# Performance work log

Hardware: AMD Instinct MI355X
Metric: run time of the kernel (lower is better)

## Reference

```python
import jax, jax.numpy as jnp
import numpy as np

N_USER = 50000
N_ITEM = 50000
E = 500000
L = 100000
F = 128
HID = 128
OUT = 64


def setup_inputs() -> dict:
    key = jax.random.key(0)
    ks = jax.random.split(key, 21)

    def ei(k, n_src, n_dst, n):
        return jnp.stack([
            jax.random.randint(jax.random.fold_in(k, 0), (n,), 0, n_src, dtype=jnp.int32),
            jax.random.randint(jax.random.fold_in(k, 1), (n,), 0, n_dst, dtype=jnp.int32),
        ])

    s1 = 1.0 / np.sqrt(F)
    s2 = 1.0 / np.sqrt(HID)
    inp = {
        "x_user": jax.random.normal(ks[0], (N_USER, F), jnp.float32),
        "x_item": jax.random.normal(ks[1], (N_ITEM, F), jnp.float32),
        "W1_src": jax.random.normal(ks[2], (3, F, HID), jnp.float32) * s1,
        "W1_dst": jax.random.normal(ks[3], (3, F, HID), jnp.float32) * s1,
        "a1_src": jax.random.normal(ks[4], (3, HID), jnp.float32) * s2,
        "a1_dst": jax.random.normal(ks[5], (3, HID), jnp.float32) * s2,
        "b1": jax.random.normal(ks[6], (3, HID), jnp.float32) * 0.01,
        "W2_src": jax.random.normal(ks[7], (3, HID, OUT), jnp.float32) * s2,
        "W2_dst": jax.random.normal(ks[8], (3, HID, OUT), jnp.float32) * s2,
        "a2_src": jax.random.normal(ks[9], (3, OUT), jnp.float32) * (1.0 / np.sqrt(OUT)),
        "a2_dst": jax.random.normal(ks[10], (3, OUT), jnp.float32) * (1.0 / np.sqrt(OUT)),
        "b2": jax.random.normal(ks[11], (3, OUT), jnp.float32) * 0.01,
        "rel_w": jax.random.normal(ks[12], (3, OUT), jnp.float32),
        "ei_rates": ei(ks[13], N_USER, N_ITEM, E),
        "ei_rev": ei(ks[14], N_ITEM, N_USER, E),
        "ei_follows": ei(ks[15], N_USER, N_USER, E),
        "eli_rates": ei(ks[16], N_USER, N_ITEM, L),
        "eli_rev": ei(ks[17], N_ITEM, N_USER, L),
        "eli_follows": ei(ks[18], N_USER, N_USER, L),
    }
    return inp


def _leaky(x):
    return jnp.where(x > 0, x, 0.2 * x)


def _gat(x_src, x_dst, ei, Ws, Wd, a_s, a_d, b, n_dst):
    # Single-head GATConv: linear src/dst, additive attention, segment softmax over dst.
    h_src = x_src @ Ws          # [Ns, C]
    h_dst = x_dst @ Wd          # [Nd, C]
    src, dst = ei[0], ei[1]
    logits = _leaky((h_src @ a_s)[src] + (h_dst @ a_d)[dst])  # [E]
    m = jax.ops.segment_max(logits, dst, num_segments=n_dst)
    m = jnp.where(jnp.isfinite(m), m, 0.0)
    ex = jnp.exp(logits - m[dst])
    den = jax.ops.segment_sum(ex, dst, num_segments=n_dst)
    alpha = ex / (den[dst] + 1e-16)
    out = jax.ops.segment_sum(alpha[:, None] * h_src[src], dst, num_segments=n_dst)
    return out + b


def reference(x_user, x_item, W1_src, W1_dst, a1_src, a1_dst, b1,
              W2_src, W2_dst, a2_src, a2_dst, b2, rel_w,
              ei_rates, ei_rev, ei_follows, eli_rates, eli_rev, eli_follows):
    # Layer 1 (HeteroConv sums contributions into each dst node type)
    h_item = _gat(x_user, x_item, ei_rates, W1_src[0], W1_dst[0], a1_src[0], a1_dst[0], b1[0], N_ITEM)
    h_user = (_gat(x_item, x_user, ei_rev, W1_src[1], W1_dst[1], a1_src[1], a1_dst[1], b1[1], N_USER)
              + _gat(x_user, x_user, ei_follows, W1_src[2], W1_dst[2], a1_src[2], a1_dst[2], b1[2], N_USER))
    h_item = jax.nn.relu(h_item)
    h_user = jax.nn.relu(h_user)
    # Layer 2
    o_item = _gat(h_user, h_item, ei_rates, W2_src[0], W2_dst[0], a2_src[0], a2_dst[0], b2[0], N_ITEM)
    o_user = (_gat(h_item, h_user, ei_rev, W2_src[1], W2_dst[1], a2_src[1], a2_dst[1], b2[1], N_USER)
              + _gat(h_user, h_user, ei_follows, W2_src[2], W2_dst[2], a2_src[2], a2_dst[2], b2[2], N_USER))
    # Bilinear edge scoring per relation
    p0 = jnp.sum(o_user[eli_rates[0]] * rel_w[0] * o_item[eli_rates[1]], axis=-1)
    p1 = jnp.sum(o_item[eli_rev[0]] * rel_w[1] * o_user[eli_rev[1]], axis=-1)
    p2 = jnp.sum(o_user[eli_follows[0]] * rel_w[2] * o_user[eli_follows[1]], axis=-1)
    return jnp.stack([p0, p1, p2])  # [3, L]
```

## Files before the change

kernel.cpp:

```cpp
#include <hip/hip_runtime.h>
#include <cstdint>
#include <cstddef>

#define N_NODE 50000
#define NEDGE  500000
#define NL     100000
#define FDIM   128
#define HIDD   128
#define OUTD   64
#define NBSC   98
#define NB     49
#define BCH    8192
#define NBP1   62

typedef unsigned int uint32;
typedef unsigned short ushort16;
typedef __attribute__((ext_vector_type(8))) short bf16x8;
typedef __attribute__((ext_vector_type(4))) float f32x4;

__device__ __forceinline__ float leakyf(float x) { return x > 0.f ? x : 0.2f * x; }

__device__ __forceinline__ uint32 bf16r(float x) {
    uint32 u = __float_as_uint(x);
    return (u + 0x7fffu + ((u >> 16) & 1u)) >> 16;
}
__device__ __forceinline__ float bf_lo(uint32 u) { return __uint_as_float(u << 16); }
__device__ __forceinline__ float bf_hi(uint32 u) { return __uint_as_float(u & 0xffff0000u); }

__global__ void fold_wd(const float* __restrict__ W1d, const float* __restrict__ a1d,
                        const float* __restrict__ W2d, const float* __restrict__ a2d,
                        float* __restrict__ wd1, float* __restrict__ wd2) {
    int r = blockIdx.x;
    int f = threadIdx.x;
    const float* w  = W1d + ((size_t)r * FDIM + f) * HIDD;
    const float* a  = a1d + r * HIDD;
    float s = 0.f;
    for (int h = 0; h < HIDD; ++h) s += w[h] * a[h];
    wd1[r * FDIM + f] = s;
    const float* w2 = W2d + ((size_t)r * HIDD + f) * OUTD;
    const float* a2 = a2d + r * OUTD;
    float s2 = 0.f;
    for (int o = 0; o < OUTD; ++o) s2 += w2[o] * a2[o];
    wd2[r * HIDD + f] = s2;
}

__global__ void wt_k(const float* __restrict__ W1s, const float* __restrict__ W2s,
                     ushort16* __restrict__ WT1, ushort16* __restrict__ WT2) {
    int idx = blockIdx.x * 256 + threadIdx.x;
    if (blockIdx.y == 0) {
        if (idx < 3 * FDIM * HIDD) {
            int k = idx & 127, n = (idx >> 7) & 127, r = idx >> 14;
            WT1[idx] = (ushort16)bf16r(W1s[((size_t)r * FDIM + k) * HIDD + n]);
        }
    } else {
        if (idx < 3 * HIDD * OUTD) {
            int k = idx & 127, n = (idx >> 7) & 63, r = idx >> 13;
            WT2[idx] = (ushort16)bf16r(W2s[((size_t)r * HIDD + k) * OUTD + n]);
        }
    }
}


__global__ __launch_bounds__(256) void part_hist(const int* __restrict__ e0,
                                                 const int* __restrict__ e1,
                                                 const int* __restrict__ e2,
                                                 int* __restrict__ bh) {
    int r = blockIdx.y, t = threadIdx.x;
    const int* ei  = (r == 0) ? e0 : (r == 1) ? e1 : e2;
    const int* dst = ei + NEDGE;
    __shared__ int lh[NB];
    if (t < NB) lh[t] = 0;
    __syncthreads();
    int base = blockIdx.x * BCH;
    int lim  = base + BCH; if (lim > NEDGE) lim = NEDGE;
    for (int i = base + t; i < lim; i += 256)
        atomicAdd(&lh[dst[i] >> 10], 1);
    __syncthreads();
    if (t < NB) bh[((size_t)r * NB + t) * NBP1 + blockIdx.x] = lh[t];
}

__global__ __launch_bounds__(256) void part_scan(int* __restrict__ bh,
                                                 int* __restrict__ bkbase) {
    int r = blockIdx.x, t = threadIdx.x;
    int* a = bh + (size_t)r * NB * NBP1;
    const int n = NB * NBP1;
    const int per = (n + 255) / 256;
    int lo = t * per, hi = lo + per; if (hi > n) hi = n;
    int s = 0;
    for (int i = lo; i < hi; ++i) s += a[i];
    __shared__ int sm[256];
    sm[t] = s;
    __syncthreads();
    for (int off = 1; off < 256; off <<= 1) {
        int x = (t >= off) ? sm[t - off] : 0;
        __syncthreads();
        sm[t] += x;
        __syncthreads();
    }
    int run = sm[t] - s;
    for (int i = lo; i < hi; ++i) { int c = a[i]; a[i] = run; run += c; }
    __syncthreads();
    if (t < NB) bkbase[r * (NB + 1) + t] = a[t * NBP1];
    if (t == NB) bkbase[r * (NB + 1) + NB] = NEDGE;
}

__global__ __launch_bounds__(256) void part_scatter(const int* __restrict__ e0,
                                                    const int* __restrict__ e1,
                                                    const int* __restrict__ e2,
                                                    const int* __restrict__ bh,
                                                    int2* __restrict__ bucketed) {
    int r = blockIdx.y, t = threadIdx.x;
    const int* ei  = (r == 0) ? e0 : (r == 1) ? e1 : e2;
    const int* dst = ei + NEDGE;
    __shared__ int cur[NB];
    if (t < NB) cur[t] = bh[((size_t)r * NB + t) * NBP1 + blockIdx.x];
    __syncthreads();
    int2* bk = bucketed + (size_t)r * NEDGE;
    int base = blockIdx.x * BCH;
    int lim  = base + BCH; if (lim > NEDGE) lim = NEDGE;
    for (int i = base + t; i < lim; i += 256) {
        int d = dst[i], s_ = ei[i];
        int pos = atomicAdd(&cur[d >> 10], 1);
        bk[pos] = make_int2(s_, d);
    }
}

__global__ __launch_bounds__(256) void bucket_count(const int2* __restrict__ bucketed,
                                                    const int* __restrict__ bkbase,
                                                    int* __restrict__ counts_all) {
    int r = blockIdx.y, k = blockIdx.x, t = threadIdx.x;
    int s0 = bkbase[r * (NB + 1) + k], s1 = bkbase[r * (NB + 1) + k + 1];
    __shared__ int lh[1024];
#pragma unroll
    for (int i = 0; i < 4; ++i) lh[t + i * 256] = 0;
    __syncthreads();
    const int2* bk = bucketed + (size_t)r * NEDGE;
    for (int i = s0 + t; i < s1; i += 256)
        atomicAdd(&lh[bk[i].y & 1023], 1);
    __syncthreads();
    int gbase = k << 10;
    int* cnt = counts_all + (size_t)r * N_NODE;
#pragma unroll
    for (int i = 0; i < 4; ++i) {
        int idx = t + i * 256;
        if (gbase + idx < N_NODE) cnt[gbase + idx] = lh[idx];
    }
}

__global__ __launch_bounds__(256) void scan1(const int* __restrict__ counts_all,
                                             int* __restrict__ bsum) {
    int r = blockIdx.y, b = blockIdx.x, t = threadIdx.x;
    int base = b * 512;
    int lim = N_NODE - base; if (lim > 512) lim = 512;
    const int* c = counts_all + (size_t)r * N_NODE + base;
    int v0 = (2 * t     < lim) ? c[2 * t]     : 0;
    int v1 = (2 * t + 1 < lim) ? c[2 * t + 1] : 0;
    __shared__ int sm[256];
    sm[t] = v0 + v1;
    __syncthreads();
    for (int off = 128; off; off >>= 1) {
        if (t < off) sm[t] += sm[t + off];
        __syncthreads();
    }
    if (t == 0) bsum[r * NBSC + b] = sm[0];
}

__global__ __launch_bounds__(256) void scan3(const int* __restrict__ counts_all,
                                             int* __restrict__ rowptr_all,
                                             const int* __restrict__ bsum) {
    int r = blockIdx.y, b = blockIdx.x, t = threadIdx.x;
    __shared__ int sm[256];
    sm[t] = (t < b) ? bsum[r * NBSC + t] : 0;
    __syncthreads();
    for (int off = 128; off; off >>= 1) {
        if (t < off) sm[t] += sm[t + off];
        __syncthreads();
    }
    int boff = sm[0];
    __syncthreads();

    int base = b * 512;
    int lim = N_NODE - base; if (lim > 512) lim = 512;
    const int* c = counts_all + (size_t)r * N_NODE;
    int* rp = rowptr_all + (size_t)r * (N_NODE + 1);
    int i0 = base + 2 * t, i1 = i0 + 1;
    int v0 = (2 * t     < lim) ? c[i0] : 0;
    int v1 = (2 * t + 1 < lim) ? c[i1] : 0;
    int ps = v0 + v1;
    sm[t] = ps;
    __syncthreads();
    for (int off = 1; off < 256; off <<= 1) {
        int x = (t >= off) ? sm[t - off] : 0;
        __syncthreads();
        sm[t] += x;
        __syncthreads();
    }
    int excl = sm[t] - ps + boff;
    if (2 * t < lim)     rp[i0] = excl;
    if (2 * t + 1 < lim) rp[i1] = excl + v0;
    if (b == 0 && t == 0) rp[N_NODE] = NEDGE;
}

__global__ __launch_bounds__(256) void bucket_scatter(const int2* __restrict__ bucketed,
                                                      const int* __restrict__ bkbase,
                                                      const int* __restrict__ rowptr_all,
                                                      int* __restrict__ srcs_all) {
    int r = blockIdx.y, k = blockIdx.x, t = threadIdx.x;
    int s0 = bkbase[r * (NB + 1) + k], s1 = bkbase[r * (NB + 1) + k + 1];
    int gbase = k << 10;
    const int* rp = rowptr_all + (size_t)r * (N_NODE + 1);
    __shared__ int cur[1024];
#pragma unroll
    for (int i = 0; i < 4; ++i) {
        int idx = t + i * 256;
        cur[idx] = (gbase + idx < N_NODE) ? rp[gbase + idx] : 0;
    }
    __syncthreads();
    const int2* bk = bucketed + (size_t)r * NEDGE;
    int* out = srcs_all + (size_t)r * NEDGE;
    for (int i = s0 + t; i < s1; i += 256) {
        int2 e = bk[i];
        int pos = atomicAdd(&cur[e.y & 1023], 1);
        out[pos] = e.x;
    }
}

template <int BN, bool RELU, bool DOT>
__global__ __launch_bounds__(256) void gemm_mfma(const float* __restrict__ A0,
                                                 const float* __restrict__ A1,
                                                 const float* __restrict__ A2,
                                                 const ushort16* __restrict__ WTbase,
                                                 const float* __restrict__ avec_base,
                                                 ushort16* __restrict__ Cbase,
                                                 float* __restrict__ al_base,
                                                 const float* __restrict__ wdvec,
                                                 float* __restrict__ adst_base, int M) {
    constexpr int K = 128;
    __shared__ ushort16 aslds[64 * K];
    __shared__ ushort16 bslds[BN * K];
    const int r = blockIdx.y;
    const float* A = (r == 0) ? A0 : (r == 1) ? A1 : A2;
    const int t    = threadIdx.x;
    const int lane = t & 63;
    const int w    = t >> 6;
    const int m0   = blockIdx.x * 64;

    {
        const uint4* src = reinterpret_cast<const uint4*>(WTbase + (size_t)r * BN * K);
        char* bb = reinterpret_cast<char*>(bslds);
#pragma unroll
        for (int i = t; i < BN * 16; i += 256) {
            int n = i >> 4, c16 = i & 15;
            uint32 off = (uint32)(n * 256 + c16 * 16) ^ (uint32)((n & 7) << 4);
            *reinterpret_cast<uint4*>(bb + off) = src[i];
        }
    }
    const float4* A4 = reinterpret_cast<const float4*>(A);
    const int mr = (r == 0) ? 1 : (r == 1) ? 0 : 2;
    const float* wdot = wdvec + mr * K;
    char* ab = reinterpret_cast<char*>(aslds);
    float dp[8];
#pragma unroll
    for (int i = 0; i < 8; ++i) dp[i] = 0.f;
#pragma unroll
    for (int i = 0; i < 8; ++i) {
        int idx = t + i * 256;
        int row = idx >> 5, kq = idx & 31;
        float4 v = make_float4(0.f, 0.f, 0.f, 0.f);
        if (m0 + row < M) {
            v = A4[(size_t)(m0 + row) * 32 + kq];
            if (RELU) {
                v.x = fmaxf(v.x, 0.f); v.y = fmaxf(v.y, 0.f);
                v.z = fmaxf(v.z, 0.f); v.w = fmaxf(v.w, 0.f);
            }
        }
        if (DOT) {
            float4 wv = *reinterpret_cast<const float4*>(&wdot[kq * 4]);
            dp[i] = fmaf(v.x, wv.x, dp[i]); dp[i] = fmaf(v.y, wv.y, dp[i]);
            dp[i] = fmaf(v.z, wv.z, dp[i]); dp[i] = fmaf(v.w, wv.w, dp[i]);
        }
        uint2 p;
        p.x = bf16r(v.x) | (bf16r(v.y) << 16);
        p.y = bf16r(v.z) | (bf16r(v.w) << 16);
        uint32 off = (uint32)(row * 256 + kq * 8) ^ (uint32)((row & 7) << 4);
        *reinterpret_cast<uint2*>(ab + off) = p;
    }
    if (DOT) {
        float* adst = adst_base + (size_t)mr * M;
#pragma unroll
        for (int i = 0; i < 8; ++i) {
            float p = dp[i];
            p += __shfl_xor(p, 16); p += __shfl_xor(p, 8); p += __shfl_xor(p, 4);
            p += __shfl_xor(p, 2);  p += __shfl_xor(p, 1);
            int row = (t + i * 256) >> 5;
            if ((t & 31) == 0 && m0 + row < M) adst[m0 + row] = p;
        }
    }
    __syncthreads();

    const int col0 = lane & 15;
    const int kgrp = lane >> 4;
    const int arow = w * 16 + col0;
    bf16x8 afrag[4];
#pragma unroll
    for (int ks = 0; ks < 4; ++ks) {
        uint32 off = (uint32)(arow * 256 + ks * 64 + kgrp * 16) ^ (uint32)((arow & 7) << 4);
        afrag[ks] = *reinterpret_cast<const bf16x8*>(ab + off);
    }
    constexpr int NT = BN / 16;
    f32x4 acc[NT];
#pragma unroll
    for (int n = 0; n < NT; ++n) acc[n] = (f32x4){0.f, 0.f, 0.f, 0.f};
    const char* bb = reinterpret_cast<const char*>(bslds);
#pragma unroll
    for (int n = 0; n < NT; ++n) {
        int bcol = n * 16 + col0;
        uint32 xw = (uint32)((bcol & 7) << 4);
#pragma unroll
        for (int ks = 0; ks < 4; ++ks) {
            uint32 off = (uint32)(bcol * 256 + ks * 64 + kgrp * 16) ^ xw;
            bf16x8 bfrag = *reinterpret_cast<const bf16x8*>(bb + off);
            acc[n] = __builtin_amdgcn_mfma_f32_16x16x32_bf16(afrag[ks], bfrag, acc[n], 0, 0, 0);
        }
    }

    ushort16* C = Cbase + (size_t)r * M * BN;
    const float* av = avec_base + r * BN;
    const int rbase = m0 + w * 16 + kgrp * 4;
    float p4[4] = {0.f, 0.f, 0.f, 0.f};
#pragma unroll
    for (int n = 0; n < NT; ++n) {
        float asv = av[n * 16 + col0];
#pragma unroll
        for (int reg = 0; reg < 4; ++reg) {
            int rr = rbase + reg;
            if (rr < M) C[(size_t)rr * BN + n * 16 + col0] = (ushort16)bf16r(acc[n][reg]);
            p4[reg] = fmaf(acc[n][reg], asv, p4[reg]);
        }
    }
    float* al = al_base + (size_t)r * M;
#pragma unroll
    for (int reg = 0; reg < 4; ++reg) {
        float q = p4[reg];
        q += __shfl_xor(q, 1); q += __shfl_xor(q, 2);
        q += __shfl_xor(q, 4); q += __shfl_xor(q, 8);
        int rr = rbase + reg;
        if (col0 == 0 && rr < M) al[rr] = q;
    }
}

__device__ __forceinline__ float4 seg128p(const int* __restrict__ rp, const int* __restrict__ ss,
                                          const float* __restrict__ als,
                                          const uint2* __restrict__ hv2,
                                          float ad, int d, int half, int col) {
    int s = rp[d], e = rp[d + 1];
    float den = 0.f;
    float4 ac = make_float4(0.f, 0.f, 0.f, 0.f);
    int i = s;
    for (; i + 4 <= e; i += 4) {
        int sA = ss[i + half];
        int sB = ss[i + 2 + half];
        float lA = als[sA], lB = als[sB];
        uint2 uA = hv2[(size_t)sA * 32 + col];
        uint2 uB = hv2[(size_t)sB * 32 + col];
        float eA = __expf(leakyf(lA + ad));
        float eB = __expf(leakyf(lB + ad));
        den += eA + eB;
        ac.x = fmaf(eA, bf_lo(uA.x), ac.x); ac.y = fmaf(eA, bf_hi(uA.x), ac.y);
        ac.z = fmaf(eA, bf_lo(uA.y), ac.z); ac.w = fmaf(eA, bf_hi(uA.y), ac.w);
        ac.x = fmaf(eB, bf_lo(uB.x), ac.x); ac.y = fmaf(eB, bf_hi(uB.x), ac.y);
        ac.z = fmaf(eB, bf_lo(uB.y), ac.z); ac.w = fmaf(eB, bf_hi(uB.y), ac.w);
    }
    if (i + 2 <= e) {
        int sA = ss[i + half];
        float lA = als[sA];
        uint2 uA = hv2[(size_t)sA * 32 + col];
        float eA = __expf(leakyf(lA + ad));
        den += eA;
        ac.x = fmaf(eA, bf_lo(uA.x), ac.x); ac.y = fmaf(eA, bf_hi(uA.x), ac.y);
        ac.z = fmaf(eA, bf_lo(uA.y), ac.z); ac.w = fmaf(eA, bf_hi(uA.y), ac.w);
        i += 2;
    }
    if (i < e && half == 0) {
        int sA = ss[i];
        float lA = als[sA];
        uint2 uA = hv2[(size_t)sA * 32 + col];
        float eA = __expf(leakyf(lA + ad));
        den += eA;
        ac.x = fmaf(eA, bf_lo(uA.x), ac.x); ac.y = fmaf(eA, bf_hi(uA.x), ac.y);
        ac.z = fmaf(eA, bf_lo(uA.y), ac.z); ac.w = fmaf(eA, bf_hi(uA.y), ac.w);
    }
    den  += __shfl_xor(den, 32);
    ac.x += __shfl_xor(ac.x, 32); ac.y += __shfl_xor(ac.y, 32);
    ac.z += __shfl_xor(ac.z, 32); ac.w += __shfl_xor(ac.w, 32);
    float rden = 1.0f / (den + 1e-16f);
    return make_float4(ac.x * rden, ac.y * rden, ac.z * rden, ac.w * rden);
}

__device__ __forceinline__ float2 seg64p(const int* __restrict__ rp, const int* __restrict__ ss,
                                         const float* __restrict__ als,
                                         const uint32* __restrict__ hv,
                                         float ad, int d, int half, int col) {
    int s = rp[d], e = rp[d + 1];
    float den = 0.f, ax = 0.f, ay = 0.f;
    int i = s;
    for (; i + 4 <= e; i += 4) {
        int sA = ss[i + half];
        int sB = ss[i + 2 + half];
        float lA = als[sA], lB = als[sB];
        uint32 uA = hv[(size_t)sA * 32 + col];
        uint32 uB = hv[(size_t)sB * 32 + col];
        float eA = __expf(leakyf(lA + ad));
        float eB = __expf(leakyf(lB + ad));
        den += eA + eB;
        ax = fmaf(eA, bf_lo(uA), ax); ay = fmaf(eA, bf_hi(uA), ay);
        ax = fmaf(eB, bf_lo(uB), ax); ay = fmaf(eB, bf_hi(uB), ay);
    }
    if (i + 2 <= e) {
        int sA = ss[i + half];
        float lA = als[sA];
        uint32 uA = hv[(size_t)sA * 32 + col];
        float eA = __expf(leakyf(lA + ad));
        den += eA;
        ax = fmaf(eA, bf_lo(uA), ax); ay = fmaf(eA, bf_hi(uA), ay);
        i += 2;
    }
    if (i < e && half == 0) {
        int sA = ss[i];
        float lA = als[sA];
        uint32 uA = hv[(size_t)sA * 32 + col];
        float eA = __expf(leakyf(lA + ad));
        den += eA;
        ax = fmaf(eA, bf_lo(uA), ax); ay = fmaf(eA, bf_hi(uA), ay);
    }
    den += __shfl_xor(den, 32);
    ax  += __shfl_xor(ax, 32);
    ay  += __shfl_xor(ay, 32);
    float rden = 1.0f / (den + 1e-16f);
    return make_float2(ax * rden, ay * rden);
}

__global__ __launch_bounds__(256) void agg1_sp(const int* __restrict__ rowptr_all,
                                               const int* __restrict__ srcs_all,
                                               const float* __restrict__ alsrc_all,
                                               float* __restrict__ aldst_all,
                                               const ushort16* __restrict__ hs_all,
                                               const float* __restrict__ b1,
                                               const float* __restrict__ wd2,
                                               float* __restrict__ h_item,
                                               float* __restrict__ h_user) {
    const int lane = threadIdx.x & 63;
    const int d = blockIdx.x * 4 + (threadIdx.x >> 6);
    if (d >= N_NODE) return;
    const int half = lane >> 5, col = lane & 31;
    const uint2* hv2 = reinterpret_cast<const uint2*>(hs_all);
    if (blockIdx.y == 0) {
        float4 w = seg128p(rowptr_all, srcs_all, alsrc_all, hv2, aldst_all[d], d, half, col);
        float4 b = ((const float4*)b1)[col];
        float4 h = make_float4(w.x + b.x, w.y + b.y, w.z + b.z, w.w + b.w);
        if (half == 0) ((float4*)h_item)[(size_t)d * 32 + col] = h;
        float4 v0 = ((const float4*)wd2)[col];
        float p = fmaxf(h.x, 0.f) * v0.x + fmaxf(h.y, 0.f) * v0.y
                + fmaxf(h.z, 0.f) * v0.z + fmaxf(h.w, 0.f) * v0.w;
        p += __shfl_xor(p, 16); p += __shfl_xor(p, 8);
        p += __shfl_xor(p, 4);  p += __shfl_xor(p, 2); p += __shfl_xor(p, 1);
        if (lane == 0) aldst_all[d] = p;
    } else {
        float4 w1 = seg128p(rowptr_all + (N_NODE + 1), srcs_all + NEDGE,
                            alsrc_all + N_NODE, hv2 + (size_t)N_NODE * 32,
                            aldst_all[N_NODE + d], d, half, col);
        float4 w2 = seg128p(rowptr_all + 2 * (N_NODE + 1), srcs_all + (size_t)2 * NEDGE,
                            alsrc_all + 2 * N_NODE, hv2 + (size_t)2 * N_NODE * 32,
                            aldst_all[2 * N_NODE + d], d, half, col);
        float4 bA = ((const float4*)(b1 + HIDD))[col];
        float4 bB = ((const float4*)(b1 + 2 * HIDD))[col];
        float4 h = make_float4(w1.x + w2.x + bA.x + bB.x, w1.y + w2.y + bA.y + bB.y,
                               w1.z + w2.z + bA.z + bB.z, w1.w + w2.w + bA.w + bB.w);
        if (half == 0) ((float4*)h_user)[(size_t)d * 32 + col] = h;
        float hx = fmaxf(h.x, 0.f), hy = fmaxf(h.y, 0.f);
        float hz = fmaxf(h.z, 0.f), hw = fmaxf(h.w, 0.f);
        float4 v1 = ((const float4*)(wd2 + HIDD))[col];
        float4 v2 = ((const float4*)(wd2 + 2 * HIDD))[col];
        float p1 = hx * v1.x + hy * v1.y + hz * v1.z + hw * v1.w;
        float p2 = hx * v2.x + hy * v2.y + hz * v2.z + hw * v2.w;
        p1 += __shfl_xor(p1, 16); p1 += __shfl_xor(p1, 8);
        p1 += __shfl_xor(p1, 4);  p1 += __shfl_xor(p1, 2); p1 += __shfl_xor(p1, 1);
        p2 += __shfl_xor(p2, 16); p2 += __shfl_xor(p2, 8);
        p2 += __shfl_xor(p2, 4);  p2 += __shfl_xor(p2, 2); p2 += __shfl_xor(p2, 1);
        if (lane == 0) {
            aldst_all[N_NODE + d]     = p1;
            aldst_all[2 * N_NODE + d] = p2;
        }
    }
}

__global__ __launch_bounds__(256) void agg2_sp(const int* __restrict__ rowptr_all,
                                               const int* __restrict__ srcs_all,
                                               const float* __restrict__ alsrc_all,
                                               const float* __restrict__ aldst_all,
                                               const ushort16* __restrict__ hs_all,
                                               const float* __restrict__ b2,
                                               float* __restrict__ o_item,
                                               float* __restrict__ o_user) {
    const int lane = threadIdx.x & 63;
    const int d = blockIdx.x * 4 + (threadIdx.x >> 6);
    if (d >= N_NODE) return;
    const int half = lane >> 5, col = lane & 31;
    const uint32* hv = reinterpret_cast<const uint32*>(hs_all);
    if (blockIdx.y == 0) {
        float2 w = seg64p(rowptr_all, srcs_all, alsrc_all, hv, aldst_all[d], d, half, col);
        float2 b = ((const float2*)b2)[col];
        if (half == 0)
            ((float2*)o_item)[(size_t)d * 32 + col] = make_float2(w.x + b.x, w.y + b.y);
    } else {
        float2 w1 = seg64p(rowptr_all + (N_NODE + 1), srcs_all + NEDGE,
                           alsrc_all + N_NODE, hv + (size_t)N_NODE * 32,
                           aldst_all[N_NODE + d], d, half, col);
        float2 w2 = seg64p(rowptr_all + 2 * (N_NODE + 1), srcs_all + (size_t)2 * NEDGE,
                           alsrc_all + 2 * N_NODE, hv + (size_t)2 * N_NODE * 32,
                           aldst_all[2 * N_NODE + d], d, half, col);
        float2 bA = ((const float2*)(b2 + OUTD))[col];
        float2 bB = ((const float2*)(b2 + 2 * OUTD))[col];
        if (half == 0)
            ((float2*)o_user)[(size_t)d * 32 + col] =
                make_float2(w1.x + w2.x + bA.x + bB.x, w1.y + w2.y + bA.y + bB.y);
    }
}

__global__ void score_k(const int* __restrict__ e0, const int* __restrict__ e1,
                        const int* __restrict__ e2,
                        const float* __restrict__ o_user, const float* __restrict__ o_item,
                        const float* __restrict__ relw, float* __restrict__ out, int L) {
    int g    = blockIdx.x * 4 + (threadIdx.x >> 6);
    int lane = threadIdx.x & 63;
    int r = g / L, l = g - r * L;
    if (r >= 3) return;
    const int* ei = (r == 0) ? e0 : (r == 1) ? e1 : e2;
    int ai = ei[l];
    int bi = ei[L + l];
    const float* A = (r == 1) ? o_item : o_user;
    const float* B = (r == 0) ? o_item : o_user;
    float v = A[(size_t)ai * OUTD + lane] * relw[r * OUTD + lane] * B[(size_t)bi * OUTD + lane];
#pragma unroll
    for (int off = 32; off; off >>= 1) v += __shfl_xor(v, off);
    if (lane == 0) out[r * L + l] = v;
}

extern "C" void kernel_launch(void* const* d_in, const int* in_sizes, int n_in,
                              void* d_out, int out_size, void* d_ws, size_t ws_size,
                              hipStream_t stream) {
    const float* x_user = (const float*)d_in[0];
    const float* x_item = (const float*)d_in[1];
    const float* W1s = (const float*)d_in[2];
    const float* W1d = (const float*)d_in[3];
    const float* a1s = (const float*)d_in[4];
    const float* a1d = (const float*)d_in[5];
    const float* b1  = (const float*)d_in[6];
    const float* W2s = (const float*)d_in[7];
    const float* W2d = (const float*)d_in[8];
    const float* a2s = (const float*)d_in[9];
    const float* a2d = (const float*)d_in[10];
    const float* b2  = (const float*)d_in[11];
    const float* relw= (const float*)d_in[12];
    const int* ei0 = (const int*)d_in[13];
    const int* ei1 = (const int*)d_in[14];
    const int* ei2 = (const int*)d_in[15];
    const int* el0 = (const int*)d_in[16];
    const int* el1 = (const int*)d_in[17];
    const int* el2 = (const int*)d_in[18];
    float* out = (float*)d_out;
    (void)ws_size; (void)n_in; (void)in_sizes; (void)out_size;

    char* ws = (char*)d_ws;
    size_t off = 0;
    auto alloc = [&](size_t bytes) -> void* {
        void* p = ws + off;
        off = (off + bytes + 255) & ~(size_t)255;
        return p;
    };
    int*     rowptr_all = (int*)alloc((size_t)3 * (N_NODE + 1) * 4);
    int*     counts_all = (int*)alloc((size_t)3 * N_NODE * 4);
    int*     srcs_all   = (int*)alloc((size_t)3 * NEDGE * 4);
    int*     bsum       = (int*)alloc((size_t)3 * NBSC * 4);
    int*     bh         = (int*)alloc((size_t)3 * NB * NBP1 * 4);
    int*     bkbase     = (int*)alloc((size_t)3 * (NB + 1) * 4);
    int2*    bucketed   = (int2*)alloc((size_t)3 * NEDGE * 8);
    ushort16* hs_bf     = (ushort16*)alloc((size_t)3 * N_NODE * HIDD * 2);
    ushort16* WT1       = (ushort16*)alloc((size_t)3 * HIDD * FDIM * 2);
    ushort16* WT2       = (ushort16*)alloc((size_t)3 * OUTD * HIDD * 2);
    float*   h_item1    = (float*)alloc((size_t)2 * N_NODE * HIDD * 4);
    float*   h_user1    = h_item1 + (size_t)N_NODE * HIDD;
    float*   o_item     = (float*)alloc((size_t)N_NODE * OUTD * 4);
    float*   o_user     = (float*)alloc((size_t)N_NODE * OUTD * 4);
    float*   alsrc_all  = (float*)alloc((size_t)3 * N_NODE * 4);
    float*   aldst_all  = (float*)alloc((size_t)3 * N_NODE * 4);
    float*   wd1        = (float*)alloc(3 * FDIM * 4);
    float*   wd2        = (float*)alloc(3 * HIDD * 4);

    fold_wd<<<3, 128, 0, stream>>>(W1d, a1d, W2d, a2d, wd1, wd2);
    wt_k<<<dim3(192, 2), 256, 0, stream>>>(W1s, W2s, WT1, WT2);

    part_hist<<<dim3(NBP1, 3), 256, 0, stream>>>(ei0, ei1, ei2, bh);
    part_scan<<<3, 256, 0, stream>>>(bh, bkbase);
    part_scatter<<<dim3(NBP1, 3), 256, 0, stream>>>(ei0, ei1, ei2, bh, bucketed);
    bucket_count<<<dim3(NB, 3), 256, 0, stream>>>(bucketed, bkbase, counts_all);
    scan1<<<dim3(NBSC, 3), 256, 0, stream>>>(counts_all, bsum);
    scan3<<<dim3(NBSC, 3), 256, 0, stream>>>(counts_all, rowptr_all, bsum);
    bucket_scatter<<<dim3(NB, 3), 256, 0, stream>>>(bucketed, bkbase, rowptr_all, srcs_all);

    const int ag = (N_NODE + 3) / 4;
    const int gg = (N_NODE + 63) / 64;

    gemm_mfma<128, false, true><<<dim3(gg, 3), 256, 0, stream>>>(
        x_user, x_item, x_user, WT1, a1s, hs_bf, alsrc_all, wd1, aldst_all, N_NODE);
    agg1_sp<<<dim3(ag, 2), 256, 0, stream>>>(rowptr_all, srcs_all, alsrc_all, aldst_all,
                                             hs_bf, b1, wd2, h_item1, h_user1);

    gemm_mfma<64, true, false><<<dim3(gg, 3), 256, 0, stream>>>(
        h_user1, h_item1, h_user1, WT2, a2s, hs_bf, alsrc_all, wd2, aldst_all, N_NODE);
    agg2_sp<<<dim3(ag, 2), 256, 0, stream>>>(rowptr_all, srcs_all, alsrc_all, aldst_all,
                                             hs_bf, b2, o_item, o_user);

    score_k<<<(3 * NL + 3) / 4, 256, 0, stream>>>(el0, el1, el2, o_user, o_item, relw, out, NL);
}
```

Before: 331.7 us.

## Store intermediate activations in bf16 and pack bucketed edges into 32 bits

The layer-1 outputs (h_item1/h_user1) and the layer-2 outputs (o_item/o_user) are now written as bf16 instead of fp32. The second GEMM reads the bf16 activations directly and applies ReLU on the packed bits, and the score kernel converts bf16 back to float. Edge bucketing packs the source index and the low 10 bits of the destination into one 32-bit word instead of an int2. Together these halve the global memory traffic in several memory-bound stages, at the cost of extra rounding in the final outputs.

```diff
diff --git a/kernel.cpp b/kernel.cpp
--- a/kernel.cpp
+++ b/kernel.cpp
@@ -18,6 +18,8 @@
 typedef __attribute__((ext_vector_type(8))) short bf16x8;
 typedef __attribute__((ext_vector_type(4))) float f32x4;
 
+static_assert(N_NODE < 65536, "src packs into 16 bits");
+
 __device__ __forceinline__ float leakyf(float x) { return x > 0.f ? x : 0.2f * x; }
 
 __device__ __forceinline__ uint32 bf16r(float x) {
@@ -26,6 +28,12 @@
 }
 __device__ __forceinline__ float bf_lo(uint32 u) { return __uint_as_float(u << 16); }
 __device__ __forceinline__ float bf_hi(uint32 u) { return __uint_as_float(u & 0xffff0000u); }
+__device__ __forceinline__ uint32 relu_bf2(uint32 u) {
+    uint32 lo = u & 0xFFFFu, hi = u >> 16;
+    lo = (lo & 0x8000u) ? 0u : lo;
+    hi = (hi & 0x8000u) ? 0u : hi;
+    return lo | (hi << 16);
+}
 
 __global__ void fold_wd(const float* __restrict__ W1d, const float* __restrict__ a1d,
                         const float* __restrict__ W2d, const float* __restrict__ a2d,
@@ -108,24 +116,24 @@
                                                     const int* __restrict__ e1,
                                                     const int* __restrict__ e2,
                                                     const int* __restrict__ bh,
-                                                    int2* __restrict__ bucketed) {
+                                                    uint32* __restrict__ bucketed) {
     int r = blockIdx.y, t = threadIdx.x;
     const int* ei  = (r == 0) ? e0 : (r == 1) ? e1 : e2;
     const int* dst = ei + NEDGE;
     __shared__ int cur[NB];
     if (t < NB) cur[t] = bh[((size_t)r * NB + t) * NBP1 + blockIdx.x];
     __syncthreads();
-    int2* bk = bucketed + (size_t)r * NEDGE;
+    uint32* bk = bucketed + (size_t)r * NEDGE;
     int base = blockIdx.x * BCH;
     int lim  = base + BCH; if (lim > NEDGE) lim = NEDGE;
     for (int i = base + t; i < lim; i += 256) {
         int d = dst[i], s_ = ei[i];
         int pos = atomicAdd(&cur[d >> 10], 1);
-        bk[pos] = make_int2(s_, d);
-    }
-}
-
-__global__ __launch_bounds__(256) void bucket_count(const int2* __restrict__ bucketed,
+        bk[pos] = (uint32)s_ | ((uint32)(d & 1023) << 16);
+    }
+}
+
+__global__ __launch_bounds__(256) void bucket_count(const uint32* __restrict__ bucketed,
                                                     const int* __restrict__ bkbase,
                                                     int* __restrict__ counts_all) {
     int r = blockIdx.y, k = blockIdx.x, t = threadIdx.x;
@@ -134,9 +142,9 @@
 #pragma unroll
     for (int i = 0; i < 4; ++i) lh[t + i * 256] = 0;
     __syncthreads();
-    const int2* bk = bucketed + (size_t)r * NEDGE;
+    const uint32* bk = bucketed + (size_t)r * NEDGE;
     for (int i = s0 + t; i < s1; i += 256)
-        atomicAdd(&lh[bk[i].y & 1023], 1);
+        atomicAdd(&lh[bk[i] >> 16], 1);
     __syncthreads();
     int gbase = k << 10;
     int* cnt = counts_all + (size_t)r * N_NODE;
@@ -201,7 +209,7 @@
     if (b == 0 && t == 0) rp[N_NODE] = NEDGE;
 }
 
-__global__ __launch_bounds__(256) void bucket_scatter(const int2* __restrict__ bucketed,
+__global__ __launch_bounds__(256) void bucket_scatter(const uint32* __restrict__ bucketed,
                                                       const int* __restrict__ bkbase,
                                                       const int* __restrict__ rowptr_all,
                                                       int* __restrict__ srcs_all) {
@@ -216,19 +224,19 @@
         cur[idx] = (gbase + idx < N_NODE) ? rp[gbase + idx] : 0;
     }
     __syncthreads();
-    const int2* bk = bucketed + (size_t)r * NEDGE;
+    const uint32* bk = bucketed + (size_t)r * NEDGE;
     int* out = srcs_all + (size_t)r * NEDGE;
     for (int i = s0 + t; i < s1; i += 256) {
-        int2 e = bk[i];
-        int pos = atomicAdd(&cur[e.y & 1023], 1);
-        out[pos] = e.x;
-    }
-}
-
-template <int BN, bool RELU, bool DOT>
-__global__ __launch_bounds__(256) void gemm_mfma(const float* __restrict__ A0,
-                                                 const float* __restrict__ A1,
-                                                 const float* __restrict__ A2,
+        uint32 e = bk[i];
+        int pos = atomicAdd(&cur[e >> 16], 1);
+        out[pos] = (int)(e & 0xFFFFu);
+    }
+}
+
+template <int BN, bool RELU, bool DOT, bool ABF16>
+__global__ __launch_bounds__(256) void gemm_mfma(const void* __restrict__ A0,
+                                                 const void* __restrict__ A1,
+                                                 const void* __restrict__ A2,
                                                  const ushort16* __restrict__ WTbase,
                                                  const float* __restrict__ avec_base,
                                                  ushort16* __restrict__ Cbase,
@@ -239,7 +247,7 @@
     __shared__ ushort16 aslds[64 * K];
     __shared__ ushort16 bslds[BN * K];
     const int r = blockIdx.y;
-    const float* A = (r == 0) ? A0 : (r == 1) ? A1 : A2;
+    const void* Av = (r == 0) ? A0 : (r == 1) ? A1 : A2;
     const int t    = threadIdx.x;
     const int lane = t & 63;
     const int w    = t >> 6;
@@ -255,45 +263,61 @@
             *reinterpret_cast<uint4*>(bb + off) = src[i];
         }
     }
-    const float4* A4 = reinterpret_cast<const float4*>(A);
-    const int mr = (r == 0) ? 1 : (r == 1) ? 0 : 2;
-    const float* wdot = wdvec + mr * K;
     char* ab = reinterpret_cast<char*>(aslds);
-    float dp[8];
-#pragma unroll
-    for (int i = 0; i < 8; ++i) dp[i] = 0.f;
-#pragma unroll
-    for (int i = 0; i < 8; ++i) {
-        int idx = t + i * 256;
-        int row = idx >> 5, kq = idx & 31;
-        float4 v = make_float4(0.f, 0.f, 0.f, 0.f);
-        if (m0 + row < M) {
-            v = A4[(size_t)(m0 + row) * 32 + kq];
-            if (RELU) {
-                v.x = fmaxf(v.x, 0.f); v.y = fmaxf(v.y, 0.f);
-                v.z = fmaxf(v.z, 0.f); v.w = fmaxf(v.w, 0.f);
+    if (ABF16) {
+        const uint2* A2v = reinterpret_cast<const uint2*>(Av);
+#pragma unroll
+        for (int i = 0; i < 8; ++i) {
+            int idx = t + i * 256;
+            int row = idx >> 5, kq = idx & 31;
+            uint2 p = make_uint2(0u, 0u);
+            if (m0 + row < M) {
+                p = A2v[(size_t)(m0 + row) * 32 + kq];
+                if (RELU) { p.x = relu_bf2(p.x); p.y = relu_bf2(p.y); }
             }
+            uint32 off = (uint32)(row * 256 + kq * 8) ^ (uint32)((row & 7) << 4);
+            *reinterpret_cast<uint2*>(ab + off) = p;
+        }
+    } else {
+        const float4* A4 = reinterpret_cast<const float4*>(Av);
+        const int mr = (r == 0) ? 1 : (r == 1) ? 0 : 2;
+        const float* wdot = wdvec + mr * K;
+        float dp[8];
+#pragma unroll
+        for (int i = 0; i < 8; ++i) dp[i] = 0.f;
+#pragma unroll
+        for (int i = 0; i < 8; ++i) {
+            int idx = t + i * 256;
+            int row = idx >> 5, kq = idx & 31;
+            float4 v = make_float4(0.f, 0.f, 0.f, 0.f);
+            if (m0 + row < M) {
+                v = A4[(size_t)(m0 + row) * 32 + kq];
+                if (RELU) {
+                    v.x = fmaxf(v.x, 0.f); v.y = fmaxf(v.y, 0.f);
+                    v.z = fmaxf(v.z, 0.f); v.w = fmaxf(v.w, 0.f);
+                }
+            }
+            if (DOT) {
+                float4 wv = *reinterpret_cast<const float4*>(&wdot[kq * 4]);
+                dp[i] = fmaf(v.x, wv.x, dp[i]); dp[i] = fmaf(v.y, wv.y, dp[i]);
+                dp[i] = fmaf(v.z, wv.z, dp[i]); dp[i] = fmaf(v.w, wv.w, dp[i]);
+            }
+            uint2 p;
+            p.x = bf16r(v.x) | (bf16r(v.y) << 16);
+            p.y = bf16r(v.z) | (bf16r(v.w) << 16);
+            uint32 off = (uint32)(row * 256 + kq * 8) ^ (uint32)((row & 7) << 4);
+            *reinterpret_cast<uint2*>(ab + off) = p;
         }
         if (DOT) {
-            float4 wv = *reinterpret_cast<const float4*>(&wdot[kq * 4]);
-            dp[i] = fmaf(v.x, wv.x, dp[i]); dp[i] = fmaf(v.y, wv.y, dp[i]);
-            dp[i] = fmaf(v.z, wv.z, dp[i]); dp[i] = fmaf(v.w, wv.w, dp[i]);
-        }
-        uint2 p;
-        p.x = bf16r(v.x) | (bf16r(v.y) << 16);
-        p.y = bf16r(v.z) | (bf16r(v.w) << 16);
-        uint32 off = (uint32)(row * 256 + kq * 8) ^ (uint32)((row & 7) << 4);
-        *reinterpret_cast<uint2*>(ab + off) = p;
-    }
-    if (DOT) {
-        float* adst = adst_base + (size_t)mr * M;
-#pragma unroll
-        for (int i = 0; i < 8; ++i) {
-            float p = dp[i];
-            p += __shfl_xor(p, 16); p += __shfl_xor(p, 8); p += __shfl_xor(p, 4);
-            p += __shfl_xor(p, 2);  p += __shfl_xor(p, 1);
-            int row = (t + i * 256) >> 5;
-            if ((t & 31) == 0 && m0 + row < M) adst[m0 + row] = p;
+            float* adst = adst_base + (size_t)mr * M;
+#pragma unroll
+            for (int i = 0; i < 8; ++i) {
+                float p = dp[i];
+                p += __shfl_xor(p, 16); p += __shfl_xor(p, 8); p += __shfl_xor(p, 4);
+                p += __shfl_xor(p, 2);  p += __shfl_xor(p, 1);
+                int row = (t + i * 256) >> 5;
+                if ((t & 31) == 0 && m0 + row < M) adst[m0 + row] = p;
+            }
         }
     }
     __syncthreads();
@@ -447,8 +471,8 @@
                                                const ushort16* __restrict__ hs_all,
                                                const float* __restrict__ b1,
                                                const float* __restrict__ wd2,
-                                               float* __restrict__ h_item,
-                                               float* __restrict__ h_user) {
+                                               ushort16* __restrict__ h_item,
+                                               ushort16* __restrict__ h_user) {
     const int lane = threadIdx.x & 63;
     const int d = blockIdx.x * 4 + (threadIdx.x >> 6);
     if (d >= N_NODE) return;
@@ -458,7 +482,12 @@
         float4 w = seg128p(rowptr_all, srcs_all, alsrc_all, hv2, aldst_all[d], d, half, col);
         float4 b = ((const float4*)b1)[col];
         float4 h = make_float4(w.x + b.x, w.y + b.y, w.z + b.z, w.w + b.w);
-        if (half == 0) ((float4*)h_item)[(size_t)d * 32 + col] = h;
+        if (half == 0) {
+            uint2 p;
+            p.x = bf16r(h.x) | (bf16r(h.y) << 16);
+            p.y = bf16r(h.z) | (bf16r(h.w) << 16);
+            ((uint2*)h_item)[(size_t)d * 32 + col] = p;
+        }
         float4 v0 = ((const float4*)wd2)[col];
         float p = fmaxf(h.x, 0.f) * v0.x + fmaxf(h.y, 0.f) * v0.y
                 + fmaxf(h.z, 0.f) * v0.z + fmaxf(h.w, 0.f) * v0.w;
@@ -476,7 +505,12 @@
         float4 bB = ((const float4*)(b1 + 2 * HIDD))[col];
         float4 h = make_float4(w1.x + w2.x + bA.x + bB.x, w1.y + w2.y + bA.y + bB.y,
                                w1.z + w2.z + bA.z + bB.z, w1.w + w2.w + bA.w + bB.w);
-        if (half == 0) ((float4*)h_user)[(size_t)d * 32 + col] = h;
+        if (half == 0) {
+            uint2 p;
+            p.x = bf16r(h.x) | (bf16r(h.y) << 16);
+            p.y = bf16r(h.z) | (bf16r(h.w) << 16);
+            ((uint2*)h_user)[(size_t)d * 32 + col] = p;
+        }
         float hx = fmaxf(h.x, 0.f), hy = fmaxf(h.y, 0.f);
         float hz = fmaxf(h.z, 0.f), hw = fmaxf(h.w, 0.f);
         float4 v1 = ((const float4*)(wd2 + HIDD))[col];
@@ -500,8 +534,8 @@
                                                const float* __restrict__ aldst_all,
                                                const ushort16* __restrict__ hs_all,
                                                const float* __restrict__ b2,
-                                               float* __restrict__ o_item,
-                                               float* __restrict__ o_user) {
+                                               ushort16* __restrict__ o_item,
+                                               ushort16* __restrict__ o_user) {
     const int lane = threadIdx.x & 63;
     const int d = blockIdx.x * 4 + (threadIdx.x >> 6);
     if (d >= N_NODE) return;
@@ -511,7 +545,8 @@
         float2 w = seg64p(rowptr_all, srcs_all, alsrc_all, hv, aldst_all[d], d, half, col);
         float2 b = ((const float2*)b2)[col];
         if (half == 0)
-            ((float2*)o_item)[(size_t)d * 32 + col] = make_float2(w.x + b.x, w.y + b.y);
+            ((uint32*)o_item)[(size_t)d * 32 + col] =
+                bf16r(w.x + b.x) | (bf16r(w.y + b.y) << 16);
     } else {
         float2 w1 = seg64p(rowptr_all + (N_NODE + 1), srcs_all + NEDGE,
                            alsrc_all + N_NODE, hv + (size_t)N_NODE * 32,
@@ -522,14 +557,14 @@
         float2 bA = ((const float2*)(b2 + OUTD))[col];
         float2 bB = ((const float2*)(b2 + 2 * OUTD))[col];
         if (half == 0)
-            ((float2*)o_user)[(size_t)d * 32 + col] =
-                make_float2(w1.x + w2.x + bA.x + bB.x, w1.y + w2.y + bA.y + bB.y);
+            ((uint32*)o_user)[(size_t)d * 32 + col] =
+                bf16r(w1.x + w2.x + bA.x + bB.x) | (bf16r(w1.y + w2.y + bA.y + bB.y) << 16);
     }
 }
 
 __global__ void score_k(const int* __restrict__ e0, const int* __restrict__ e1,
                         const int* __restrict__ e2,
-                        const float* __restrict__ o_user, const float* __restrict__ o_item,
+                        const ushort16* __restrict__ o_user, const ushort16* __restrict__ o_item,
                         const float* __restrict__ relw, float* __restrict__ out, int L) {
     int g    = blockIdx.x * 4 + (threadIdx.x >> 6);
     int lane = threadIdx.x & 63;
@@ -538,9 +573,11 @@
     const int* ei = (r == 0) ? e0 : (r == 1) ? e1 : e2;
     int ai = ei[l];
     int bi = ei[L + l];
-    const float* A = (r == 1) ? o_item : o_user;
-    const float* B = (r == 0) ? o_item : o_user;
-    float v = A[(size_t)ai * OUTD + lane] * relw[r * OUTD + lane] * B[(size_t)bi * OUTD + lane];
+    const ushort16* A = (r == 1) ? o_item : o_user;
+    const ushort16* B = (r == 0) ? o_item : o_user;
+    float av = __uint_as_float(((uint32)A[(size_t)ai * OUTD + lane]) << 16);
+    float bv = __uint_as_float(((uint32)B[(size_t)bi * OUTD + lane]) << 16);
+    float v = av * relw[r * OUTD + lane] * bv;
 #pragma unroll
     for (int off = 32; off; off >>= 1) v += __shfl_xor(v, off);
     if (lane == 0) out[r * L + l] = v;
@@ -584,14 +621,14 @@
     int*     bsum       = (int*)alloc((size_t)3 * NBSC * 4);
     int*     bh         = (int*)alloc((size_t)3 * NB * NBP1 * 4);
     int*     bkbase     = (int*)alloc((size_t)3 * (NB + 1) * 4);
-    int2*    bucketed   = (int2*)alloc((size_t)3 * NEDGE * 8);
+    uint32*  bucketed   = (uint32*)alloc((size_t)3 * NEDGE * 4);
     ushort16* hs_bf     = (ushort16*)alloc((size_t)3 * N_NODE * HIDD * 2);
     ushort16* WT1       = (ushort16*)alloc((size_t)3 * HIDD * FDIM * 2);
     ushort16* WT2       = (ushort16*)alloc((size_t)3 * OUTD * HIDD * 2);
-    float*   h_item1    = (float*)alloc((size_t)2 * N_NODE * HIDD * 4);
-    float*   h_user1    = h_item1 + (size_t)N_NODE * HIDD;
-    float*   o_item     = (float*)alloc((size_t)N_NODE * OUTD * 4);
-    float*   o_user     = (float*)alloc((size_t)N_NODE * OUTD * 4);
+    ushort16* h_item1   = (ushort16*)alloc((size_t)2 * N_NODE * HIDD * 2);
+    ushort16* h_user1   = h_item1 + (size_t)N_NODE * HIDD;
+    ushort16* o_item    = (ushort16*)alloc((size_t)N_NODE * OUTD * 2);
+    ushort16* o_user    = (ushort16*)alloc((size_t)N_NODE * OUTD * 2);
     float*   alsrc_all  = (float*)alloc((size_t)3 * N_NODE * 4);
     float*   aldst_all  = (float*)alloc((size_t)3 * N_NODE * 4);
     float*   wd1        = (float*)alloc(3 * FDIM * 4);
@@ -611,12 +648,12 @@
     const int ag = (N_NODE + 3) / 4;
     const int gg = (N_NODE + 63) / 64;
 
-    gemm_mfma<128, false, true><<<dim3(gg, 3), 256, 0, stream>>>(
+    gemm_mfma<128, false, true, false><<<dim3(gg, 3), 256, 0, stream>>>(
         x_user, x_item, x_user, WT1, a1s, hs_bf, alsrc_all, wd1, aldst_all, N_NODE);
     agg1_sp<<<dim3(ag, 2), 256, 0, stream>>>(rowptr_all, srcs_all, alsrc_all, aldst_all,
                                              hs_bf, b1, wd2, h_item1, h_user1);
 
-    gemm_mfma<64, true, false><<<dim3(gg, 3), 256, 0, stream>>>(
+    gemm_mfma<64, true, false, true><<<dim3(gg, 3), 256, 0, stream>>>(
         h_user1, h_item1, h_user1, WT2, a2s, hs_bf, alsrc_all, wd2, aldst_all, N_NODE);
     agg2_sp<<<dim3(ag, 2), 256, 0, stream>>>(rowptr_all, srcs_all, alsrc_all, aldst_all,
                                              hs_bf, b2, o_item, o_user);
```

New measurement: 329.3 us. Within noise of the previous version (-0.7%).
